# Kernel optimization log

Measured on AMD Instinct MI355X. Metric: run time of the kernel, lower is better.

## Reference

```python
import jax, jax.numpy as jnp
import numpy as np

EMBED = 512
HID = 16
BATCH = 4
SEQ = 1024


def setup_inputs() -> dict:
    key = jax.random.key(0)
    ks = jax.random.split(key, 8)
    e, h = EMBED, HID
    inputs = jax.random.normal(ks[0], (BATCH, SEQ, e), dtype=jnp.float32)
    # nn.Linear default init ~ U(-1/sqrt(fan_in), 1/sqrt(fan_in)); approximate scale
    Wq = jax.random.normal(ks[1], (e, e), dtype=jnp.float32) / np.sqrt(e)
    Wk = jax.random.normal(ks[2], (e, e), dtype=jnp.float32) / np.sqrt(e)
    Wv = jax.random.normal(ks[3], (e, e), dtype=jnp.float32) / np.sqrt(e)
    W1 = jax.random.normal(ks[4], (h, 2 * e), dtype=jnp.float32) / np.sqrt(2 * e)
    b1 = jnp.zeros((h,), dtype=jnp.float32)
    w2 = jax.random.normal(ks[5], (h,), dtype=jnp.float32) / np.sqrt(h)
    b2 = jnp.zeros((1,), dtype=jnp.float32)
    return {"inputs": inputs, "Wq": Wq, "Wk": Wk, "Wv": Wv,
            "W1": W1, "b1": b1, "w2": w2, "b2": b2}


def reference(inputs, Wq, Wk, Wv, W1, b1, w2, b2):
    e = inputs.shape[-1]
    # projections (torch Linear: x @ W.T)
    q = jnp.einsum('bse,fe->bsf', inputs, Wq)
    k = jnp.einsum('bse,fe->bsf', inputs, Wk)
    v = jnp.einsum('bse,fe->bsf', inputs, Wv)
    # attn_net Linear over concat [q_i; k_j] factorizes:
    # W1 @ [q;k] = W1[:, :e] @ q_i + W1[:, e:] @ k_j
    A = jnp.einsum('bse,he->bsh', q, W1[:, :e]) + b1  # (b, s, h)
    B = jnp.einsum('bse,he->bsh', k, W1[:, e:])       # (b, s, h)
    hidden = jnp.tanh(A[:, :, None, :] + B[:, None, :, :])  # (b, s, s, h)
    logits = jnp.einsum('bijh,h->bij', hidden, w2) + b2[0]   # (b, s, s)
    attn = jax.nn.softmax(logits, axis=-1)
    return jnp.einsum('bij,bjd->bid', attn, v)
```

## Files before the change

### kernel.cpp

```cpp
#include <hip/hip_runtime.h>
#include <math.h>
#include <stdint.h>

#define EMBED 512
#define HID 16
#define SEQ 1024

typedef unsigned short u16;
typedef __attribute__((ext_vector_type(8))) __bf16 bf16x8;
typedef __attribute__((ext_vector_type(4))) float f32x4;

__device__ __forceinline__ u16 f2bf(float f) {
    unsigned u = __float_as_uint(f);
    unsigned r = (u + 0x7FFFu + ((u >> 16) & 1u)) >> 16;
    return (u16)r;
}
__device__ __forceinline__ float bf2f(u16 h) {
    return __uint_as_float(((unsigned)h) << 16);
}
__device__ __forceinline__ void gload16(const void* g, void* d) {
    __builtin_amdgcn_global_load_lds(
        reinterpret_cast<const __attribute__((address_space(1))) unsigned int*>(
            reinterpret_cast<uintptr_t>(g)),
        reinterpret_cast<__attribute__((address_space(3))) unsigned int*>(
            reinterpret_cast<uintptr_t>(d)),
        16, 0, 0);
}

__global__ __launch_bounds__(256) void prep_kernel(
    const float* __restrict__ Wq, const float* __restrict__ Wk,
    const float* __restrict__ W1, const float* __restrict__ Wvm,
    const float* __restrict__ x,
    u16* __restrict__ AH, u16* __restrict__ AL, u16* __restrict__ x_hi)
{
    __shared__ float w1s[EMBED];
    int t = threadIdx.x;
    int blk = blockIdx.x;
    if (blk < 64) {
        int h2 = blk >> 1, half = blk & 1;
        int ab = h2 >> 4, h = h2 & 15;
        const float* Wmat = ab ? Wk : Wq;
        const float* w1row = W1 + (size_t)h * (2 * EMBED) + ab * EMBED;
        for (int f = t; f < EMBED; f += 256) w1s[f] = w1row[f];
        __syncthreads();
        int e0 = (half << 8) + t;
        float acc = 0.f;
        #pragma unroll 16
        for (int f = 0; f < EMBED; ++f)
            acc += w1s[f] * Wmat[(size_t)f * EMBED + e0];
        u16 hi = f2bf(acc);
        AH[(size_t)(512 + h2) * EMBED + e0] = hi;
        AL[(size_t)(512 + h2) * EMBED + e0] = f2bf(acc - bf2f(hi));
        AH[(size_t)(544 + h2) * EMBED + e0] = 0;
        AL[(size_t)(544 + h2) * EMBED + e0] = 0;
    } else if (blk < 320) {
        int i = (blk - 64) * 256 + t;
        float4 v = ((const float4*)Wvm)[i];
        u16 h0 = f2bf(v.x), h1 = f2bf(v.y), h2 = f2bf(v.z), h3 = f2bf(v.w);
        ((ushort4*)AH)[i] = make_ushort4(h0, h1, h2, h3);
        ((ushort4*)AL)[i] = make_ushort4(f2bf(v.x - bf2f(h0)), f2bf(v.y - bf2f(h1)),
                                         f2bf(v.z - bf2f(h2)), f2bf(v.w - bf2f(h3)));
    } else {
        int i = (blk - 320) * 256 + t;
        float4 v = ((const float4*)x)[i];
        ((ushort4*)x_hi)[i] = make_ushort4(f2bf(v.x), f2bf(v.y), f2bf(v.z), f2bf(v.w));
    }
}

template<int NR>
__device__ __forceinline__ void stageR(const u16* src, int ld, int kt,
                                       u16* ldsb, int t)
{
    int kb0 = kt << 7;
    #pragma unroll
    for (int i = 0; i < NR / 32; ++i) {
        int row  = i * 32 + (t >> 3);
        int colb = (((t & 7) ^ ((t >> 3) & 7)) << 4);
        const char* g = (const char*)src + (size_t)row * ((size_t)ld * 2) + kb0 + colb;
        gload16(g, (char*)ldsb + i * 4096 + ((t >> 6) << 10) + ((t & 63) << 4));
    }
}
__device__ __forceinline__ bf16x8 ldfrag(const u16* ldsb, int r, int s) {
    return *(const bf16x8*)((const char*)ldsb + r * 128 + (((s ^ (r & 7))) << 4));
}

__global__ __launch_bounds__(256, 4) void gemm_kernel(
    const u16* __restrict__ AH, const u16* __restrict__ AL,
    const u16* __restrict__ Bh, const float* __restrict__ b1,
    u16* __restrict__ VT, float* __restrict__ EAt, float* __restrict__ EBt)
{
    const float K2 = 2.8853900817779268f;
    constexpr int TOFF = 64 * 64;
    __shared__ __attribute__((aligned(16))) u16 lds[3 * TOFF];
    int t = threadIdx.x;
    int l = t & 63, wid = t >> 6;
    int wm = (wid >> 1) * 32, wn = (wid & 1) * 32;
    int m0 = blockIdx.y * 64, n0 = blockIdx.x * 64;
    const u16* pAh = AH + (size_t)m0 * EMBED;
    const u16* pAl = AL + (size_t)m0 * EMBED;
    const u16* pBh = Bh + (size_t)n0 * EMBED;
    f32x4 acc[2][2] = {};
    const bool two = (blockIdx.y == 8);

    if (two) {
        for (int kt = 0; kt < 8; ++kt) {
            stageR<64>(pAh, EMBED, kt, lds, t);
            stageR<64>(pAl, EMBED, kt, lds + TOFF, t);
            stageR<64>(pBh, EMBED, kt, lds + 2 * TOFF, t);
            __syncthreads();
            #pragma unroll
            for (int kk = 0; kk < 2; ++kk) {
                int sb = (kk << 2) + (l >> 4);
                bf16x8 ah[2], al2[2], bh[2];
                #pragma unroll
                for (int mf = 0; mf < 2; ++mf) {
                    int r = wm + mf * 16 + (l & 15);
                    ah[mf]  = ldfrag(lds, r, sb);
                    al2[mf] = ldfrag(lds + TOFF, r, sb);
                }
                #pragma unroll
                for (int nf = 0; nf < 2; ++nf)
                    bh[nf] = ldfrag(lds + 2 * TOFF, wn + nf * 16 + (l & 15), sb);
                #pragma unroll
                for (int mf = 0; mf < 2; ++mf)
                    #pragma unroll
                    for (int nf = 0; nf < 2; ++nf) {
                        acc[mf][nf] = __builtin_amdgcn_mfma_f32_16x16x32_bf16(ah[mf],  bh[nf], acc[mf][nf], 0, 0, 0);
                        acc[mf][nf] = __builtin_amdgcn_mfma_f32_16x16x32_bf16(al2[mf], bh[nf], acc[mf][nf], 0, 0, 0);
                    }
            }
            __syncthreads();
        }
    } else {
        for (int kt = 0; kt < 8; ++kt) {
            stageR<64>(pAh, EMBED, kt, lds, t);
            stageR<64>(pBh, EMBED, kt, lds + 2 * TOFF, t);
            __syncthreads();
            #pragma unroll
            for (int kk = 0; kk < 2; ++kk) {
                int sb = (kk << 2) + (l >> 4);
                bf16x8 ah[2], bh[2];
                #pragma unroll
                for (int mf = 0; mf < 2; ++mf)
                    ah[mf] = ldfrag(lds, wm + mf * 16 + (l & 15), sb);
                #pragma unroll
                for (int nf = 0; nf < 2; ++nf)
                    bh[nf] = ldfrag(lds + 2 * TOFF, wn + nf * 16 + (l & 15), sb);
                #pragma unroll
                for (int mf = 0; mf < 2; ++mf)
                    #pragma unroll
                    for (int nf = 0; nf < 2; ++nf)
                        acc[mf][nf] = __builtin_amdgcn_mfma_f32_16x16x32_bf16(ah[mf], bh[nf], acc[mf][nf], 0, 0, 0);
            }
            __syncthreads();
        }
    }

    int cr = (l >> 4) << 2, cc = l & 15;
    #pragma unroll
    for (int mf = 0; mf < 2; ++mf)
        #pragma unroll
        for (int nf = 0; nf < 2; ++nf)
            #pragma unroll
            for (int r = 0; r < 4; ++r) {
                int gr = m0 + wm + mf * 16 + cr + r;
                int col = n0 + wn + nf * 16 + cc;
                float v = acc[mf][nf][r];
                if (gr < 512) {
                    VT[(size_t)gr * 4096 + col] = f2bf(v);
                } else if (gr < 528) {
                    EAt[(size_t)(gr - 512) * 4096 + col] =
                        __builtin_amdgcn_exp2f(K2 * (v + b1[gr - 512]));
                } else if (gr < 544) {
                    EBt[(size_t)(gr - 528) * 4096 + col] =
                        __builtin_amdgcn_exp2f(K2 * v);
                }
            }
}

__global__ __launch_bounds__(256) void attn_kernel(
    const float* __restrict__ EAt, const float* __restrict__ EBt,
    const float* __restrict__ w2, u16* __restrict__ P)
{
    const float L2E = 1.4426950408889634f;
    __shared__ float redA[4], redB[4];
    int blk = blockIdx.x;
    int b = blk >> 9;
    int i0 = (blk & 511) << 1;
    int t = threadIdx.x;
    int gA = (b << 10) + i0;

    float ax[HID], ay[HID];
    #pragma unroll
    for (int h = 0; h < HID; ++h) {
        ax[h] = EAt[(size_t)h * 4096 + gA];
        ay[h] = EAt[(size_t)h * 4096 + gA + 1];
    }

    float P1a[8], P2a[8], PSa[8];
    #pragma unroll
    for (int p = 0; p < 8; ++p) {
        float w1 = -2.f * w2[2 * p], w2_ = -2.f * w2[2 * p + 1];
        P1a[p] = w1; P2a[p] = w2_; PSa[p] = w1 + w2_;
    }
    float S0 = 0.f;
    #pragma unroll
    for (int p = 0; p < 8; ++p) S0 += fmaxf(P1a[p], 0.f) + fmaxf(P2a[p], 0.f);

    const float* EBb = EBt + (b << 10);
    float pa0, pa1, pa2, pa3, pb0, pb1, pb2, pb3;

#define DOC(c, PA, PB) { \
    int j = t + (c) * 256; \
    float bb[HID]; \
    _Pragma("unroll") \
    for (int h = 0; h < HID; ++h) bb[h] = EBb[(size_t)h * 4096 + j]; \
    float sA = 0.f, sB = 0.f; \
    _Pragma("unroll") \
    for (int q = 0; q < 4; ++q) { \
        int h0 = q << 2, p0 = q << 1, p1 = p0 + 1; \
        { float e1 = ax[h0]*bb[h0], e2 = ax[h0+1]*bb[h0+1]; \
          float e3 = ax[h0+2]*bb[h0+2], e4 = ax[h0+3]*bb[h0+3]; \
          float D12 = fmaf(e1, e2, e1) + (e2 + 1.0f); \
          float N12 = fmaf(P2a[p0], e1, fmaf(P1a[p0], e2, PSa[p0])); \
          float D34 = fmaf(e3, e4, e3) + (e4 + 1.0f); \
          float N34 = fmaf(P2a[p1], e3, fmaf(P1a[p1], e4, PSa[p1])); \
          sA = fmaf(fmaf(N12, D34, N34 * D12), __builtin_amdgcn_rcpf(D12 * D34), sA); } \
        { float e1 = ay[h0]*bb[h0], e2 = ay[h0+1]*bb[h0+1]; \
          float e3 = ay[h0+2]*bb[h0+2], e4 = ay[h0+3]*bb[h0+3]; \
          float D12 = fmaf(e1, e2, e1) + (e2 + 1.0f); \
          float N12 = fmaf(P2a[p0], e1, fmaf(P1a[p0], e2, PSa[p0])); \
          float D34 = fmaf(e3, e4, e3) + (e4 + 1.0f); \
          float N34 = fmaf(P2a[p1], e3, fmaf(P1a[p1], e4, PSa[p1])); \
          sB = fmaf(fmaf(N12, D34, N34 * D12), __builtin_amdgcn_rcpf(D12 * D34), sB); } \
    } \
    PA = __builtin_amdgcn_exp2f((sA - S0) * L2E); \
    PB = __builtin_amdgcn_exp2f((sB - S0) * L2E); }

    DOC(0, pa0, pb0)
    DOC(1, pa1, pb1)
    DOC(2, pa2, pb2)
    DOC(3, pa3, pb3)
#undef DOC

    float sA = (pa0 + pa1) + (pa2 + pa3);
    float sB = (pb0 + pb1) + (pb2 + pb3);
    #pragma unroll
    for (int o = 32; o > 0; o >>= 1) {
        sA += __shfl_xor(sA, o);
        sB += __shfl_xor(sB, o);
    }
    if ((t & 63) == 0) { redA[t >> 6] = sA; redB[t >> 6] = sB; }
    __syncthreads();
    float invA = __fdividef(1.f, (redA[0] + redA[1]) + (redA[2] + redA[3]));
    float invB = __fdividef(1.f, (redB[0] + redB[1]) + (redB[2] + redB[3]));

    size_t baseA = ((size_t)(b * SEQ) + i0) * SEQ;
    size_t baseB = baseA + SEQ;
    P[baseA + t      ] = f2bf(pa0 * invA);
    P[baseA + t + 256] = f2bf(pa1 * invA);
    P[baseA + t + 512] = f2bf(pa2 * invA);
    P[baseA + t + 768] = f2bf(pa3 * invA);
    P[baseB + t      ] = f2bf(pb0 * invB);
    P[baseB + t + 256] = f2bf(pb1 * invB);
    P[baseB + t + 512] = f2bf(pb2 * invB);
    P[baseB + t + 768] = f2bf(pb3 * invB);
}

__global__ __launch_bounds__(256, 4) void pv_kernel(
    const u16* __restrict__ P, const u16* __restrict__ VT,
    float* __restrict__ out)
{
    constexpr int AOFF = 64 * 64;
    constexpr int BOFF = 64 * 64;
    constexpr int BUFW = AOFF + BOFF;
    __shared__ __attribute__((aligned(16))) u16 lds[2 * BUFW];
    int t = threadIdx.x;
    int l = t & 63, wid = t >> 6;
    int wm = (wid >> 1) * 32, wn = (wid & 1) * 32;
    int m0 = blockIdx.y * 64, n0 = blockIdx.x * 64;
    int zb = blockIdx.z;
    const u16* pA = P + (size_t)zb * SEQ * SEQ + (size_t)m0 * SEQ;
    const u16* pB = VT + (size_t)n0 * 4096 + ((size_t)zb << 10);

    f32x4 acc[2][2] = {};

    auto STAGE = [&](int buf, int kt) {
        u16* base = lds + buf * BUFW;
        stageR<64>(pA, SEQ, kt, base, t);
        stageR<64>(pB, 4096, kt, base + AOFF, t);
    };
    auto COMPUTE = [&](int buf) {
        u16* lA = lds + buf * BUFW;
        u16* lB = lA + AOFF;
        #pragma unroll
        for (int kk = 0; kk < 2; ++kk) {
            int sb = (kk << 2) + (l >> 4);
            bf16x8 af[2], bf_[2];
            #pragma unroll
            for (int mf = 0; mf < 2; ++mf)
                af[mf] = ldfrag(lA, wm + mf * 16 + (l & 15), sb);
            #pragma unroll
            for (int nf = 0; nf < 2; ++nf)
                bf_[nf] = ldfrag(lB, wn + nf * 16 + (l & 15), sb);
            #pragma unroll
            for (int mf = 0; mf < 2; ++mf)
                #pragma unroll
                for (int nf = 0; nf < 2; ++nf)
                    acc[mf][nf] = __builtin_amdgcn_mfma_f32_16x16x32_bf16(af[mf], bf_[nf], acc[mf][nf], 0, 0, 0);
        }
    };

    STAGE(0, 0);
    __syncthreads();
    int cur = 0;
    for (int kt = 0; kt + 1 < 16; ++kt) {
        STAGE(cur ^ 1, kt + 1);
        COMPUTE(cur);
        __syncthreads();
        cur ^= 1;
    }
    COMPUTE(cur);

    int cr = (l >> 4) << 2, cc = l & 15;
    #pragma unroll
    for (int mf = 0; mf < 2; ++mf)
        #pragma unroll
        for (int nf = 0; nf < 2; ++nf)
            #pragma unroll
            for (int r = 0; r < 4; ++r)
                out[((size_t)(zb * SEQ) + m0 + wm + mf * 16 + cr + r) * EMBED
                    + n0 + wn + nf * 16 + cc] = acc[mf][nf][r];
}

extern "C" void kernel_launch(void* const* d_in, const int* in_sizes, int n_in,
                              void* d_out, int out_size, void* d_ws, size_t ws_size,
                              hipStream_t stream) {
    const float* x   = (const float*)d_in[0];
    const float* Wq  = (const float*)d_in[1];
    const float* Wk  = (const float*)d_in[2];
    const float* Wvm = (const float*)d_in[3];
    const float* W1  = (const float*)d_in[4];
    const float* b1  = (const float*)d_in[5];
    const float* w2  = (const float*)d_in[6];

    char* ws = (char*)d_ws;
    u16*   AH   = (u16*)(ws + 0);
    u16*   AL   = (u16*)(ws + 589824);
    u16*   x_hi = (u16*)(ws + 1179648);
    u16*   VT   = (u16*)(ws + 5373952);
    float* EAt  = (float*)(ws + 9568256);
    float* EBt  = (float*)(ws + 9830400);
    u16*   P    = (u16*)(ws + 10092544);
    float* out  = (float*)d_out;

    hipLaunchKernelGGL(prep_kernel, dim3(2368), dim3(256), 0, stream,
                       Wq, Wk, W1, Wvm, x, AH, AL, x_hi);
    hipLaunchKernelGGL(gemm_kernel, dim3(64, 9), dim3(256), 0, stream,
                       AH, AL, x_hi, b1, VT, EAt, EBt);
    hipLaunchKernelGGL(attn_kernel, dim3(2048), dim3(256), 0, stream,
                       EAt, EBt, w2, P);
    hipLaunchKernelGGL(pv_kernel, dim3(8, 16, 4), dim3(256), 0, stream,
                       P, VT, out);
}
```

Measured before the change: 59.04 us.

## Double K-step per barrier and swizzle block order in GEMM and PV kernels

Both the projection GEMM and the PV GEMM now stage two 64-wide K slices per synchronisation, which halves the number of barriers and raises LDS use per block. Launch bounds drop so the larger shared buffers still fit. A linear block-index remap spreads tiles across XCDs/L2 so blocks sharing operands are grouped. The branch on the two-pass (hi/lo) row tile moves inside the unified loop. The cost is more LDS per block and lower occupancy.

```diff
diff --git a/kernel.cpp b/kernel.cpp
--- a/kernel.cpp
+++ b/kernel.cpp
@@ -84,76 +84,71 @@
     return *(const bf16x8*)((const char*)ldsb + r * 128 + (((s ^ (r & 7))) << 4));
 }
 
-__global__ __launch_bounds__(256, 4) void gemm_kernel(
+__global__ __launch_bounds__(256, 3) void gemm_kernel(
     const u16* __restrict__ AH, const u16* __restrict__ AL,
     const u16* __restrict__ Bh, const float* __restrict__ b1,
     u16* __restrict__ VT, float* __restrict__ EAt, float* __restrict__ EBt)
 {
     const float K2 = 2.8853900817779268f;
-    constexpr int TOFF = 64 * 64;
-    __shared__ __attribute__((aligned(16))) u16 lds[3 * TOFF];
+    __shared__ __attribute__((aligned(16))) u16 lds[24576];
     int t = threadIdx.x;
     int l = t & 63, wid = t >> 6;
     int wm = (wid >> 1) * 32, wn = (wid & 1) * 32;
-    int m0 = blockIdx.y * 64, n0 = blockIdx.x * 64;
+    int lin = blockIdx.y * 64 + blockIdx.x;
+    int v = (lin & 7) * 72 + (lin >> 3);
+    int mt = v % 9, nt = v / 9;
+    int m0 = mt * 64, n0 = nt * 64;
     const u16* pAh = AH + (size_t)m0 * EMBED;
     const u16* pAl = AL + (size_t)m0 * EMBED;
     const u16* pBh = Bh + (size_t)n0 * EMBED;
     f32x4 acc[2][2] = {};
-    const bool two = (blockIdx.y == 8);
-
-    if (two) {
-        for (int kt = 0; kt < 8; ++kt) {
-            stageR<64>(pAh, EMBED, kt, lds, t);
-            stageR<64>(pAl, EMBED, kt, lds + TOFF, t);
-            stageR<64>(pBh, EMBED, kt, lds + 2 * TOFF, t);
-            __syncthreads();
-            #pragma unroll
-            for (int kk = 0; kk < 2; ++kk) {
-                int sb = (kk << 2) + (l >> 4);
-                bf16x8 ah[2], al2[2], bh[2];
-                #pragma unroll
-                for (int mf = 0; mf < 2; ++mf) {
-                    int r = wm + mf * 16 + (l & 15);
-                    ah[mf]  = ldfrag(lds, r, sb);
-                    al2[mf] = ldfrag(lds + TOFF, r, sb);
-                }
-                #pragma unroll
-                for (int nf = 0; nf < 2; ++nf)
-                    bh[nf] = ldfrag(lds + 2 * TOFF, wn + nf * 16 + (l & 15), sb);
-                #pragma unroll
-                for (int mf = 0; mf < 2; ++mf)
-                    #pragma unroll
-                    for (int nf = 0; nf < 2; ++nf) {
-                        acc[mf][nf] = __builtin_amdgcn_mfma_f32_16x16x32_bf16(ah[mf],  bh[nf], acc[mf][nf], 0, 0, 0);
-                        acc[mf][nf] = __builtin_amdgcn_mfma_f32_16x16x32_bf16(al2[mf], bh[nf], acc[mf][nf], 0, 0, 0);
-                    }
-            }
-            __syncthreads();
-        }
-    } else {
-        for (int kt = 0; kt < 8; ++kt) {
-            stageR<64>(pAh, EMBED, kt, lds, t);
-            stageR<64>(pBh, EMBED, kt, lds + 2 * TOFF, t);
-            __syncthreads();
+    const bool two = (mt == 8);
+
+    for (int kp = 0; kp < 4; ++kp) {
+        stageR<64>(pAh, EMBED, 2 * kp,     lds,         t);
+        if (two) stageR<64>(pAl, EMBED, 2 * kp,     lds + 4096,  t);
+        stageR<64>(pBh, EMBED, 2 * kp,     lds + 8192,  t);
+        stageR<64>(pAh, EMBED, 2 * kp + 1, lds + 12288, t);
+        if (two) stageR<64>(pAl, EMBED, 2 * kp + 1, lds + 16384, t);
+        stageR<64>(pBh, EMBED, 2 * kp + 1, lds + 20480, t);
+        __syncthreads();
+        #pragma unroll
+        for (int half = 0; half < 2; ++half) {
+            u16* lAh = lds + half * 12288;
+            u16* lAl = lAh + 4096;
+            u16* lB  = lAh + 8192;
             #pragma unroll
             for (int kk = 0; kk < 2; ++kk) {
                 int sb = (kk << 2) + (l >> 4);
                 bf16x8 ah[2], bh[2];
                 #pragma unroll
                 for (int mf = 0; mf < 2; ++mf)
-                    ah[mf] = ldfrag(lds, wm + mf * 16 + (l & 15), sb);
+                    ah[mf] = ldfrag(lAh, wm + mf * 16 + (l & 15), sb);
                 #pragma unroll
                 for (int nf = 0; nf < 2; ++nf)
-                    bh[nf] = ldfrag(lds + 2 * TOFF, wn + nf * 16 + (l & 15), sb);
-                #pragma unroll
-                for (int mf = 0; mf < 2; ++mf)
+                    bh[nf] = ldfrag(lB, wn + nf * 16 + (l & 15), sb);
+                if (two) {
+                    bf16x8 al2[2];
                     #pragma unroll
-                    for (int nf = 0; nf < 2; ++nf)
-                        acc[mf][nf] = __builtin_amdgcn_mfma_f32_16x16x32_bf16(ah[mf], bh[nf], acc[mf][nf], 0, 0, 0);
+                    for (int mf = 0; mf < 2; ++mf)
+                        al2[mf] = ldfrag(lAl, wm + mf * 16 + (l & 15), sb);
+                    #pragma unroll
+                    for (int mf = 0; mf < 2; ++mf)
+                        #pragma unroll
+                        for (int nf = 0; nf < 2; ++nf) {
+                            acc[mf][nf] = __builtin_amdgcn_mfma_f32_16x16x32_bf16(ah[mf],  bh[nf], acc[mf][nf], 0, 0, 0);
+                            acc[mf][nf] = __builtin_amdgcn_mfma_f32_16x16x32_bf16(al2[mf], bh[nf], acc[mf][nf], 0, 0, 0);
+                        }
+                } else {
+                    #pragma unroll
+                    for (int mf = 0; mf < 2; ++mf)
+                        #pragma unroll
+                        for (int nf = 0; nf < 2; ++nf)
+                            acc[mf][nf] = __builtin_amdgcn_mfma_f32_16x16x32_bf16(ah[mf], bh[nf], acc[mf][nf], 0, 0, 0);
+                }
             }
-            __syncthreads();
         }
+        __syncthreads();
     }
 
     int cr = (l >> 4) << 2, cc = l & 15;
@@ -165,15 +160,15 @@
             for (int r = 0; r < 4; ++r) {
                 int gr = m0 + wm + mf * 16 + cr + r;
                 int col = n0 + wn + nf * 16 + cc;
-                float v = acc[mf][nf][r];
+                float v2 = acc[mf][nf][r];
                 if (gr < 512) {
-                    VT[(size_t)gr * 4096 + col] = f2bf(v);
+                    VT[(size_t)gr * 4096 + col] = f2bf(v2);
                 } else if (gr < 528) {
                     EAt[(size_t)(gr - 512) * 4096 + col] =
-                        __builtin_amdgcn_exp2f(K2 * (v + b1[gr - 512]));
+                        __builtin_amdgcn_exp2f(K2 * (v2 + b1[gr - 512]));
                 } else if (gr < 544) {
                     EBt[(size_t)(gr - 528) * 4096 + col] =
-                        __builtin_amdgcn_exp2f(K2 * v);
+                        __builtin_amdgcn_exp2f(K2 * v2);
                 }
             }
 }
@@ -267,55 +262,60 @@
     P[baseB + t + 768] = f2bf(pb3 * invB);
 }
 
-__global__ __launch_bounds__(256, 4) void pv_kernel(
+__global__ __launch_bounds__(256, 2) void pv_kernel(
     const u16* __restrict__ P, const u16* __restrict__ VT,
     float* __restrict__ out)
 {
-    constexpr int AOFF = 64 * 64;
-    constexpr int BOFF = 64 * 64;
-    constexpr int BUFW = AOFF + BOFF;
-    __shared__ __attribute__((aligned(16))) u16 lds[2 * BUFW];
+    __shared__ __attribute__((aligned(16))) u16 lds[32768];
     int t = threadIdx.x;
     int l = t & 63, wid = t >> 6;
     int wm = (wid >> 1) * 32, wn = (wid & 1) * 32;
-    int m0 = blockIdx.y * 64, n0 = blockIdx.x * 64;
-    int zb = blockIdx.z;
+    int lin = (blockIdx.z << 7) + (blockIdx.y << 3) + blockIdx.x;
+    int v = (lin & 7) * 64 + (lin >> 3);
+    int zb = v >> 7;
+    int w_ = v & 127;
+    int m0 = (w_ >> 3) * 64, n0 = (w_ & 7) * 64;
     const u16* pA = P + (size_t)zb * SEQ * SEQ + (size_t)m0 * SEQ;
     const u16* pB = VT + (size_t)n0 * 4096 + ((size_t)zb << 10);
 
     f32x4 acc[2][2] = {};
 
-    auto STAGE = [&](int buf, int kt) {
-        u16* base = lds + buf * BUFW;
-        stageR<64>(pA, SEQ, kt, base, t);
-        stageR<64>(pB, 4096, kt, base + AOFF, t);
+    auto STAGE = [&](int buf, int kp) {
+        u16* base = lds + buf * 16384;
+        stageR<64>(pA, SEQ,  2 * kp,     base,         t);
+        stageR<64>(pB, 4096, 2 * kp,     base + 4096,  t);
+        stageR<64>(pA, SEQ,  2 * kp + 1, base + 8192,  t);
+        stageR<64>(pB, 4096, 2 * kp + 1, base + 12288, t);
     };
     auto COMPUTE = [&](int buf) {
-        u16* lA = lds + buf * BUFW;
-        u16* lB = lA + AOFF;
         #pragma unroll
-        for (int kk = 0; kk < 2; ++kk) {
-            int sb = (kk << 2) + (l >> 4);
-            bf16x8 af[2], bf_[2];
+        for (int half = 0; half < 2; ++half) {
+            u16* lA = lds + buf * 16384 + half * 8192;
+            u16* lB = lA + 4096;
             #pragma unroll
-            for (int mf = 0; mf < 2; ++mf)
-                af[mf] = ldfrag(lA, wm + mf * 16 + (l & 15), sb);
-            #pragma unroll
-            for (int nf = 0; nf < 2; ++nf)
-                bf_[nf] = ldfrag(lB, wn + nf * 16 + (l & 15), sb);
-            #pragma unroll
-            for (int mf = 0; mf < 2; ++mf)
+            for (int kk = 0; kk < 2; ++kk) {
+                int sb = (kk << 2) + (l >> 4);
+                bf16x8 af[2], bf_[2];
+                #pragma unroll
+                for (int mf = 0; mf < 2; ++mf)
+                    af[mf] = ldfrag(lA, wm + mf * 16 + (l & 15), sb);
                 #pragma unroll
                 for (int nf = 0; nf < 2; ++nf)
-                    acc[mf][nf] = __builtin_amdgcn_mfma_f32_16x16x32_bf16(af[mf], bf_[nf], acc[mf][nf], 0, 0, 0);
+                    bf_[nf] = ldfrag(lB, wn + nf * 16 + (l & 15), sb);
+                #pragma unroll
+                for (int mf = 0; mf < 2; ++mf)
+                    #pragma unroll
+                    for (int nf = 0; nf < 2; ++nf)
+                        acc[mf][nf] = __builtin_amdgcn_mfma_f32_16x16x32_bf16(af[mf], bf_[nf], acc[mf][nf], 0, 0, 0);
+            }
         }
     };
 
     STAGE(0, 0);
     __syncthreads();
     int cur = 0;
-    for (int kt = 0; kt + 1 < 16; ++kt) {
-        STAGE(cur ^ 1, kt + 1);
+    for (int kp = 0; kp + 1 < 8; ++kp) {
+        STAGE(cur ^ 1, kp + 1);
         COMPUTE(cur);
         __syncthreads();
         cur ^= 1;
```

Result: faster. 54.42 us (-7.8%).
